# Kernel tuning notes

Measured on AMD Instinct MI355X. Metric: run time of the kernel, lower is better.

The kernel has to match this reference:

```python
import jax, jax.numpy as jnp
import numpy as np

KERNEL = 2  # kernel_size == stride (non-overlapping pooling, matches default stride=None)


def _pool_argmax_flat(x, k):
    """Non-overlapping k x k max-pool; returns flat H*W indices of each window max.

    Matches torch.nn.functional.max_pool2d(..., return_indices=True) for
    stride == kernel_size: first occurrence of the max in row-major window order.
    """
    B, C, H, W = x.shape
    Hp, Wp = H // k, W // k
    # (B, C, Hp, k, Wp, k) -> (B, C, Hp, Wp, k*k), window elements in row-major order
    xw = x.reshape(B, C, Hp, k, Wp, k).transpose(0, 1, 2, 4, 3, 5).reshape(B, C, Hp, Wp, k * k)
    a = jnp.argmax(xw, axis=-1)                      # (B, C, Hp, Wp), first-max like torch
    dh, dw = a // k, a % k
    rows = jnp.arange(Hp).reshape(1, 1, Hp, 1) * k + dh
    cols = jnp.arange(Wp).reshape(1, 1, 1, Wp) * k + dw
    idx = rows * W + cols                            # flat index into H*W
    return idx.reshape(B, C, Hp * Wp)                # (B, C, P)


def setup_inputs() -> dict:
    key = jax.random.key(0)
    x = jax.random.normal(key, (8, 128, 64, 64), dtype=jnp.float32)
    return {"x": x}


def reference(x) -> jnp.ndarray:
    B, C, H, W = x.shape
    idx = _pool_argmax_flat(x, KERNEL)               # (B, C_pool, P) int32
    x_flat = x.reshape(B, C, H * W)                  # (B, C_val, HW)

    def gather_one(xf, id_):
        # xf: (C_val, HW), id_: (C_pool, P)
        g = xf[:, id_]                               # (C_val, C_pool, P)
        return jnp.swapaxes(g, 0, 1)                 # (C_pool, C_val, P)

    # result[b, c_pool, c_val, i] = x_flat[b, c_val, idx[b, c_pool, i]]
    return jax.vmap(gather_one)(x_flat, idx)         # (B, C, C, P)
```

## Files before the change

### kernel.cpp

```cpp
#include <hip/hip_runtime.h>

#define BATCH 8
#define CH    128
#define HH    64
#define WW    64
#define HP    32
#define WP    32
#define NP    1024
#define PLANE 4096

__global__ __launch_bounds__(256)
void pool_gather_kernel(const float* __restrict__ x, float* __restrict__ out) {
    const int b = blockIdx.x;
    const int i = blockIdx.y;
    const int t = threadIdx.x;

    const float* planeI = x + ((size_t)(b * CH + i) << 12);

    int idx[4];
#pragma unroll
    for (int k = 0; k < 4; ++k) {
        const int p  = t + (k << 8);
        const int hp = p >> 5;
        const int wp = p & 31;
        const float2* r0 = (const float2*)(planeI + (hp << 7));
        const float2* r1 = (const float2*)(planeI + (hp << 7) + WW);
        const float2 topv = r0[wp];
        const float2 botv = r1[wp];
        float m = topv.x; int a = 0;
        if (topv.y > m) { m = topv.y; a = 1; }
        if (botv.x > m) { m = botv.x; a = 2; }
        if (botv.y > m) { m = botv.y; a = 3; }
        const int row = (hp << 1) + (a >> 1);
        const int col = (wp << 1) + (a & 1);
        idx[k] = (row << 6) + col;
    }

    const float* planeB  = x + ((size_t)(b * CH) << 12);
    float*       outBase = out + (((size_t)(b * CH + i) * CH) << 10) + t;

    for (int j = 0; j < CH; ++j) {
        const float* pj = planeB + ((size_t)j << 12);
        const float v0 = pj[idx[0]];
        const float v1 = pj[idx[1]];
        const float v2 = pj[idx[2]];
        const float v3 = pj[idx[3]];
        float* o = outBase + ((size_t)j << 10);
        o[0]   = v0;
        o[256] = v1;
        o[512] = v2;
        o[768] = v3;
    }
}

extern "C" void kernel_launch(void* const* d_in, const int* in_sizes, int n_in,
                              void* d_out, int out_size, void* d_ws, size_t ws_size,
                              hipStream_t stream) {
    const float* x  = (const float*)d_in[0];
    float*       out = (float*)d_out;
    dim3 grid(BATCH, CH);
    pool_gather_kernel<<<grid, 256, 0, stream>>>(x, out);
}
```

Measured before the change: 583.3 us.

## Stage value planes in double-buffered LDS and reuse across grouped pool channels

Each block now handles 8 pooling channels and a 32-channel chunk of value planes. Each value plane is copied into shared memory through a double buffer, then gathered for all 8 index sets. The goal is to replace scattered global/L2 gathers with LDS reads and to reuse each loaded plane eight times. The cost is 32KB of LDS per block, a barrier on every plane, more index registers (32 per thread), and a smaller grid.

```diff
diff --git a/kernel.cpp b/kernel.cpp
--- a/kernel.cpp
+++ b/kernel.cpp
@@ -2,62 +2,76 @@
 
 #define BATCH 8
 #define CH    128
-#define HH    64
-#define WW    64
-#define HP    32
-#define WP    32
-#define NP    1024
+#define G     8
+#define JC    32
 #define PLANE 4096
 
 __global__ __launch_bounds__(256)
 void pool_gather_kernel(const float* __restrict__ x, float* __restrict__ out) {
-    const int b = blockIdx.x;
-    const int i = blockIdx.y;
-    const int t = threadIdx.x;
+    __shared__ float buf[2][PLANE];
+    const int b  = blockIdx.x;
+    const int ig = blockIdx.y;
+    const int jc = blockIdx.z;
+    const int t  = threadIdx.x;
 
-    const float* planeI = x + ((size_t)(b * CH + i) << 12);
-
-    int idx[4];
+    int idx[G][4];
+    for (int g = 0; g < G; ++g) {
+        const float* planeI = x + ((size_t)(b * CH + ig * G + g) << 12);
 #pragma unroll
-    for (int k = 0; k < 4; ++k) {
-        const int p  = t + (k << 8);
-        const int hp = p >> 5;
-        const int wp = p & 31;
-        const float2* r0 = (const float2*)(planeI + (hp << 7));
-        const float2* r1 = (const float2*)(planeI + (hp << 7) + WW);
-        const float2 topv = r0[wp];
-        const float2 botv = r1[wp];
-        float m = topv.x; int a = 0;
-        if (topv.y > m) { m = topv.y; a = 1; }
-        if (botv.x > m) { m = botv.x; a = 2; }
-        if (botv.y > m) { m = botv.y; a = 3; }
-        const int row = (hp << 1) + (a >> 1);
-        const int col = (wp << 1) + (a & 1);
-        idx[k] = (row << 6) + col;
+        for (int k = 0; k < 4; ++k) {
+            const int p  = t + (k << 8);
+            const int hp = p >> 5;
+            const int wp = p & 31;
+            const float2 topv = ((const float2*)(planeI + (hp << 7)))[wp];
+            const float2 botv = ((const float2*)(planeI + (hp << 7) + 64))[wp];
+            float m = topv.x; int a = 0;
+            if (topv.y > m) { m = topv.y; a = 1; }
+            if (botv.x > m) { m = botv.x; a = 2; }
+            if (botv.y > m) { m = botv.y; a = 3; }
+            idx[g][k] = (((hp << 1) + (a >> 1)) << 6) + (wp << 1) + (a & 1);
+        }
     }
 
-    const float* planeB  = x + ((size_t)(b * CH) << 12);
-    float*       outBase = out + (((size_t)(b * CH + i) * CH) << 10) + t;
+    const float* planeB = x + ((size_t)(b * CH) << 12);
+    const int j0 = jc * JC;
 
-    for (int j = 0; j < CH; ++j) {
-        const float* pj = planeB + ((size_t)j << 12);
-        const float v0 = pj[idx[0]];
-        const float v1 = pj[idx[1]];
-        const float v2 = pj[idx[2]];
-        const float v3 = pj[idx[3]];
-        float* o = outBase + ((size_t)j << 10);
-        o[0]   = v0;
-        o[256] = v1;
-        o[512] = v2;
-        o[768] = v3;
+    {
+        const float4* src = (const float4*)(planeB + ((size_t)j0 << 12));
+        float4* dst = (float4*)buf[0];
+#pragma unroll
+        for (int c = 0; c < 4; ++c) dst[t + (c << 8)] = src[t + (c << 8)];
+    }
+
+    for (int jj = 0; jj < JC; ++jj) {
+        __syncthreads();
+        const int cur = jj & 1;
+        if (jj + 1 < JC) {
+            const float4* src = (const float4*)(planeB + ((size_t)(j0 + jj + 1) << 12));
+            float4* dst = (float4*)buf[cur ^ 1];
+#pragma unroll
+            for (int c = 0; c < 4; ++c) dst[t + (c << 8)] = src[t + (c << 8)];
+        }
+        const float* bp = buf[cur];
+#pragma unroll
+        for (int g = 0; g < G; ++g) {
+            const float v0 = bp[idx[g][0]];
+            const float v1 = bp[idx[g][1]];
+            const float v2 = bp[idx[g][2]];
+            const float v3 = bp[idx[g][3]];
+            float* o = out + (((size_t)((b * CH + ig * G + g) * CH + j0 + jj)) << 10) + t;
+            o[0]   = v0;
+            o[256] = v1;
+            o[512] = v2;
+            o[768] = v3;
+        }
     }
 }
 
 extern "C" void kernel_launch(void* const* d_in, const int* in_sizes, int n_in,
                               void* d_out, int out_size, void* d_ws, size_t ws_size,
                               hipStream_t stream) {
-    const float* x  = (const float*)d_in[0];
+    const float* x   = (const float*)d_in[0];
     float*       out = (float*)d_out;
-    dim3 grid(BATCH, CH);
+    dim3 grid(BATCH, CH / G, CH / JC);
     pool_gather_kernel<<<grid, 256, 0, stream>>>(x, out);
 }
```

Result: faster. 558.7 us (-4.2%).
